# Optimization experiments

Hardware: AMD Instinct MI355X
Metric: run time of the kernel (lower is better)

Reference implementation:

```python
import jax, jax.numpy as jnp
import numpy as np

EMBED_DIM = 1024
NUM_HEADS = 16
HEAD_DIM = EMBED_DIM // NUM_HEADS


def setup_inputs() -> dict:
    key = jax.random.key(0)
    k1, k2, k3, k4 = jax.random.split(key, 4)
    scale = 1.0 / np.sqrt(EMBED_DIM)
    x = jax.random.normal(k1, (2, 2048, EMBED_DIM), dtype=jnp.float32)
    Wqkv = jax.random.normal(k2, (3 * EMBED_DIM, EMBED_DIM), dtype=jnp.float32) * scale
    Wproj = jax.random.normal(k3, (EMBED_DIM, EMBED_DIM), dtype=jnp.float32) * scale
    bproj = jax.random.normal(k4, (EMBED_DIM,), dtype=jnp.float32) * 0.01
    return {"x": x, "Wqkv": Wqkv, "Wproj": Wproj, "bproj": bproj}


def reference(x, Wqkv, Wproj, bproj):
    B, T, D = x.shape
    # QKV projection (torch Linear: x @ W.T), no bias
    qkv = jnp.einsum('btd,ed->bte', x, Wqkv)              # [B, T, 3D]
    qkv = qkv.reshape(B, T, 3, NUM_HEADS, HEAD_DIM)
    qkv = jnp.transpose(qkv, (2, 0, 3, 1, 4))             # [3, B, H, T, hd]
    q, k, v = qkv[0], qkv[1], qkv[2]
    # scaled dot-product attention (full matrix, as in source)
    dots = jnp.einsum('bhqd,bhkd->bhqk', q, k) / jnp.sqrt(jnp.asarray(HEAD_DIM, x.dtype))
    attn = jax.nn.softmax(dots, axis=-1)
    out = jnp.einsum('bhqk,bhkd->bhqd', attn, v)          # [B, H, T, hd]
    out = jnp.transpose(out, (0, 2, 1, 3)).reshape(B, T, D)
    # output projection with bias
    return jnp.einsum('btd,ed->bte', out, Wproj) + bproj
```

## Files before the change

### kernel.cpp

```cpp
#include <hip/hip_runtime.h>

typedef __attribute__((ext_vector_type(8))) short bf16x8;
typedef __attribute__((ext_vector_type(4))) float f32x4;
typedef __attribute__((ext_vector_type(4))) unsigned int u32x4;

#define MFMA16(a, b, c) __builtin_amdgcn_mfma_f32_16x16x32_bf16((a), (b), (c), 0, 0, 0)

__device__ __forceinline__ unsigned short f2bf(float f) {
    unsigned u = __builtin_bit_cast(unsigned, f);
    u = (u + 0x7fffu + ((u >> 16) & 1u)) >> 16;
    return (unsigned short)u;
}

__device__ __forceinline__ unsigned pack2(float lo, float hi) {
    return (unsigned)f2bf(lo) | ((unsigned)f2bf(hi) << 16);
}

__device__ __forceinline__ void gll16(const void* g, void* l) {
    __builtin_amdgcn_global_load_lds((__attribute__((address_space(1))) void*)g,
                                     (__attribute__((address_space(3))) void*)l,
                                     16, 0, 0);
}

__global__ __launch_bounds__(256) void castk(const float* __restrict__ in,
                                             unsigned short* __restrict__ out, int n) {
    int stride = gridDim.x * blockDim.x;
    for (int i = blockIdx.x * blockDim.x + threadIdx.x; i * 4 < n; i += stride) {
        float4 v = ((const float4*)in)[i];
        ushort4 o;
        o.x = f2bf(v.x); o.y = f2bf(v.y); o.z = f2bf(v.z); o.w = f2bf(v.w);
        ((ushort4*)out)[i] = o;
    }
}

template <int EPI>
__global__ __launch_bounds__(256) void gemm_bt(const unsigned short* __restrict__ A,
                                               const unsigned short* __restrict__ B,
                                               int K,
                                               unsigned short* __restrict__ qbuf,
                                               unsigned short* __restrict__ kbuf,
                                               unsigned short* __restrict__ vtb,
                                               float* __restrict__ outF,
                                               const float* __restrict__ bias) {
    __shared__ __align__(16) unsigned short As[128 * 32];
    __shared__ __align__(16) unsigned short Bs[128 * 32];
    const int tid = threadIdx.x;
    const int w = tid >> 6, l = tid & 63;
    const int g = l >> 4, cc = l & 15;
    const int wr = w >> 1, wc = w & 1;
    const int m0 = blockIdx.y * 128, n0 = blockIdx.x * 128;

    f32x4 acc[4][4];
#pragma unroll
    for (int i = 0; i < 4; ++i)
#pragma unroll
        for (int j = 0; j < 4; ++j) acc[i][j] = (f32x4){0.f, 0.f, 0.f, 0.f};

    const int srow = (l >> 2);
    const int skk = (l & 3) * 8;

    for (int k0 = 0; k0 < K; k0 += 32) {
#pragma unroll
        for (int ch = 0; ch < 2; ++ch) {
            int ci = ch * 4 + w;
            int row = ci * 16 + srow;
            gll16(A + (size_t)(m0 + row) * K + k0 + skk, &As[ci * 512]);
            gll16(B + (size_t)(n0 + row) * K + k0 + skk, &Bs[ci * 512]);
        }
        __syncthreads();
        bf16x8 af[4], bfr[4];
#pragma unroll
        for (int i = 0; i < 4; ++i) {
            af[i]  = *(const bf16x8*)&As[(wr * 64 + i * 16 + cc) * 32 + g * 8];
            bfr[i] = *(const bf16x8*)&Bs[(wc * 64 + i * 16 + cc) * 32 + g * 8];
        }
#pragma unroll
        for (int i = 0; i < 4; ++i)
#pragma unroll
            for (int j = 0; j < 4; ++j) acc[i][j] = MFMA16(af[i], bfr[j], acc[i][j]);
        __syncthreads();
    }

    if (EPI == 0) {
        const int which = n0 >> 10;
#pragma unroll
        for (int jn = 0; jn < 4; ++jn) {
            int n = n0 + wc * 64 + jn * 16 + cc;
            int hn = n & 1023;
            int h = hn >> 6, d = hn & 63;
#pragma unroll
            for (int i = 0; i < 4; ++i) {
#pragma unroll
                for (int j = 0; j < 4; ++j) {
                    int m = m0 + wr * 64 + i * 16 + g * 4 + j;
                    int b = m >> 11, t = m & 2047;
                    int bh = b * 16 + h;
                    float v = acc[i][jn][j];
                    if (which == 0) {
                        qbuf[((size_t)bh * 2048 + t) * 64 + d] = f2bf(v * 0.125f);
                    } else if (which == 1) {
                        kbuf[((size_t)bh * 2048 + t) * 64 + d] = f2bf(v);
                    } else {
                        vtb[((size_t)bh * 64 + d) * 2048 + t] = f2bf(v);
                    }
                }
            }
        }
    } else {
#pragma unroll
        for (int jn = 0; jn < 4; ++jn) {
            int n = n0 + wc * 64 + jn * 16 + cc;
            float bn = bias[n];
#pragma unroll
            for (int i = 0; i < 4; ++i) {
#pragma unroll
                for (int j = 0; j < 4; ++j) {
                    int m = m0 + wr * 64 + i * 16 + g * 4 + j;
                    outF[(size_t)m * 1024 + n] = acc[i][jn][j] + bn;
                }
            }
        }
    }
}

__global__ __launch_bounds__(256) void attn_kernel(const unsigned short* __restrict__ qb,
                                                   const unsigned short* __restrict__ kb,
                                                   const unsigned short* __restrict__ vtb,
                                                   unsigned short* __restrict__ ao) {
    __shared__ __align__(16) unsigned short smem[16384];
    const int bh = blockIdx.y;
    const int w = threadIdx.x >> 6, l = threadIdx.x & 63;
    const int g = l >> 4, cc = l & 15;
    const int q0 = blockIdx.x * 128 + w * 32;

    const unsigned short* qbase = qb + (size_t)bh * 2048 * 64;
    const unsigned short* kbase = kb + (size_t)bh * 2048 * 64;
    const unsigned short* vbase = vtb + (size_t)bh * 64 * 2048;

    const int sl8 = l >> 3, sl7 = l & 7;
    const int sperm = ((sl7 ^ sl8) * 8);

#define STAGE(bb, kk)                                                                        \
    do {                                                                                     \
        int base = (bb) * 8192;                                                              \
        gll16(kbase + (size_t)((kk) + w * 8 + sl8) * 64 + sperm, &smem[base + w * 512]);     \
        gll16(kbase + (size_t)((kk) + (w + 4) * 8 + sl8) * 64 + sperm,                       \
              &smem[base + (w + 4) * 512]);                                                  \
        gll16(vbase + (size_t)(w * 8 + sl8) * 2048 + (kk) + sperm,                           \
              &smem[base + 4096 + w * 512]);                                                 \
        gll16(vbase + (size_t)((w + 4) * 8 + sl8) * 2048 + (kk) + sperm,                     \
              &smem[base + 4096 + (w + 4) * 512]);                                           \
    } while (0)

    bf16x8 qf[2][2];
#pragma unroll
    for (int qt = 0; qt < 2; ++qt)
#pragma unroll
        for (int kh = 0; kh < 2; ++kh)
            qf[qt][kh] = *(const bf16x8*)(qbase + (size_t)(q0 + qt * 16 + cc) * 64 + kh * 32 + g * 8);

    float mrun[2] = {-INFINITY, -INFINITY};
    float lrun[2] = {0.f, 0.f};
    f32x4 acc[2][4];
#pragma unroll
    for (int qt = 0; qt < 2; ++qt)
#pragma unroll
        for (int dt = 0; dt < 4; ++dt) acc[qt][dt] = (f32x4){0.f, 0.f, 0.f, 0.f};

    const int swz = cc & 7;
    const int slo = (g & 1) * 32 + cc, shi = slo + 16;

    STAGE(0, 0);
    asm volatile("s_waitcnt vmcnt(0)" ::: "memory");
    __syncthreads();

    for (int t = 0; t < 32; ++t) {
        const int cb = t & 1;
        if (t + 1 < 32) STAGE(cb ^ 1, (t + 1) * 64);

        const unsigned short* Kb = &smem[cb * 8192];
        const unsigned short* Vb = &smem[cb * 8192 + 4096];

        bf16x8 kf[4][2];
#pragma unroll
        for (int kt = 0; kt < 4; ++kt)
#pragma unroll
            for (int kh = 0; kh < 2; ++kh)
                kf[kt][kh] = *(const bf16x8*)&Kb[(kt * 16 + cc) * 64 + (((kh * 4 + g) ^ swz) * 8)];

        f32x4 s[2][4];
#pragma unroll
        for (int qt = 0; qt < 2; ++qt)
#pragma unroll
            for (int kt = 0; kt < 4; ++kt) {
                f32x4 z = (f32x4){0.f, 0.f, 0.f, 0.f};
                z = MFMA16(kf[kt][0], qf[qt][0], z);
                z = MFMA16(kf[kt][1], qf[qt][1], z);
                s[qt][kt] = z;
            }

        u32x4 pf[2][2];
#pragma unroll
        for (int qt = 0; qt < 2; ++qt) {
            float mc = s[qt][0][0];
#pragma unroll
            for (int kt = 0; kt < 4; ++kt)
#pragma unroll
                for (int j = 0; j < 4; ++j) mc = fmaxf(mc, s[qt][kt][j]);
            mc = fmaxf(mc, __shfl_xor(mc, 16));
            mc = fmaxf(mc, __shfl_xor(mc, 32));
            float mnew = fmaxf(mrun[qt], mc);
            float fsc = __expf(mrun[qt] - mnew);
            mrun[qt] = mnew;
            float p[4][4], sum = 0.f;
#pragma unroll
            for (int kt = 0; kt < 4; ++kt)
#pragma unroll
                for (int j = 0; j < 4; ++j) {
                    p[kt][j] = __expf(s[qt][kt][j] - mnew);
                    sum += p[kt][j];
                }
            lrun[qt] = lrun[qt] * fsc + sum;
#pragma unroll
            for (int dt = 0; dt < 4; ++dt) acc[qt][dt] = acc[qt][dt] * fsc;

#pragma unroll
            for (int c = 0; c < 2; ++c) {
                unsigned b0 = pack2(p[2 * c][0], p[2 * c][1]);
                unsigned b1 = pack2(p[2 * c][2], p[2 * c][3]);
                unsigned b2 = pack2(p[2 * c + 1][0], p[2 * c + 1][1]);
                unsigned b3 = pack2(p[2 * c + 1][2], p[2 * c + 1][3]);
                unsigned a0 = (unsigned)__shfl((int)b0, slo), a1 = (unsigned)__shfl((int)b1, slo);
                unsigned a2 = (unsigned)__shfl((int)b0, shi), a3 = (unsigned)__shfl((int)b1, shi);
                unsigned d0 = (unsigned)__shfl((int)b2, slo), d1 = (unsigned)__shfl((int)b3, slo);
                unsigned d2 = (unsigned)__shfl((int)b2, shi), d3 = (unsigned)__shfl((int)b3, shi);
                u32x4 wv;
                if (g < 2) { wv.x = a0; wv.y = a1; wv.z = a2; wv.w = a3; }
                else       { wv.x = d0; wv.y = d1; wv.z = d2; wv.w = d3; }
                pf[qt][c] = wv;
            }
        }

#pragma unroll
        for (int c = 0; c < 2; ++c)
#pragma unroll
            for (int dt = 0; dt < 4; ++dt) {
                bf16x8 vf = *(const bf16x8*)&Vb[(dt * 16 + cc) * 64 + (((c * 4 + g) ^ swz) * 8)];
                acc[0][dt] = MFMA16(vf, __builtin_bit_cast(bf16x8, pf[0][c]), acc[0][dt]);
                acc[1][dt] = MFMA16(vf, __builtin_bit_cast(bf16x8, pf[1][c]), acc[1][dt]);
            }

        asm volatile("s_waitcnt vmcnt(0)" ::: "memory");
        __syncthreads();
    }
#undef STAGE

    const int b = bh >> 4, h = bh & 15;
#pragma unroll
    for (int qt = 0; qt < 2; ++qt) {
        float lsum = lrun[qt];
        lsum += __shfl_xor(lsum, 16);
        lsum += __shfl_xor(lsum, 32);
        float inv = 1.f / lsum;
        size_t rowbase = ((size_t)(b * 2048 + q0 + qt * 16 + cc)) * 1024 + h * 64;
#pragma unroll
        for (int dt = 0; dt < 4; ++dt)
#pragma unroll
            for (int j = 0; j < 4; ++j)
                ao[rowbase + dt * 16 + g * 4 + j] = f2bf(acc[qt][dt][j] * inv);
    }
}

extern "C" void kernel_launch(void* const* d_in, const int* in_sizes, int n_in,
                              void* d_out, int out_size, void* d_ws, size_t ws_size,
                              hipStream_t stream) {
    const float* x = (const float*)d_in[0];
    const float* Wqkv = (const float*)d_in[1];
    const float* Wproj = (const float*)d_in[2];
    const float* bproj = (const float*)d_in[3];
    float* out = (float*)d_out;

    unsigned short* xb = (unsigned short*)d_ws;
    unsigned short* wqkvb = xb + 4096 * 1024;
    unsigned short* wprojb = wqkvb + 3072 * 1024;
    unsigned short* qbuf = wprojb + 1024 * 1024;
    unsigned short* kbuf = qbuf + 32 * 2048 * 64;
    unsigned short* vtb = kbuf + 32 * 2048 * 64;
    unsigned short* aob = vtb + 32 * 2048 * 64;

    castk<<<1024, 256, 0, stream>>>(x, xb, 4096 * 1024);
    castk<<<1024, 256, 0, stream>>>(Wqkv, wqkvb, 3072 * 1024);
    castk<<<512, 256, 0, stream>>>(Wproj, wprojb, 1024 * 1024);

    gemm_bt<0><<<dim3(24, 32), 256, 0, stream>>>(xb, wqkvb, 1024, qbuf, kbuf, vtb, nullptr, nullptr);
    attn_kernel<<<dim3(16, 32), 256, 0, stream>>>(qbuf, kbuf, vtb, aob);
    gemm_bt<1><<<dim3(8, 32), 256, 0, stream>>>(aob, wprojb, 1024, nullptr, nullptr, nullptr, out, bproj);
}
```

Before: 231.5 us.

## Double-buffer GEMM loads, swizzle tile order, streamline attention softmax and PV MFMAs

```diff
diff --git a/kernel.cpp b/kernel.cpp
--- a/kernel.cpp
+++ b/kernel.cpp
@@ -1,10 +1,12 @@
 #include <hip/hip_runtime.h>
 
 typedef __attribute__((ext_vector_type(8))) short bf16x8;
+typedef __attribute__((ext_vector_type(4))) short bf16x4;
 typedef __attribute__((ext_vector_type(4))) float f32x4;
-typedef __attribute__((ext_vector_type(4))) unsigned int u32x4;
-
-#define MFMA16(a, b, c) __builtin_amdgcn_mfma_f32_16x16x32_bf16((a), (b), (c), 0, 0, 0)
+typedef __attribute__((ext_vector_type(2))) unsigned int u32x2;
+
+#define MFMA32(a, b, c) __builtin_amdgcn_mfma_f32_16x16x32_bf16((a), (b), (c), 0, 0, 0)
+#define MFMA16K(a, b, c) __builtin_amdgcn_mfma_f32_16x16x16bf16_1k((a), (b), (c), 0, 0, 0)
 
 __device__ __forceinline__ unsigned short f2bf(float f) {
     unsigned u = __builtin_bit_cast(unsigned, f);
@@ -12,8 +14,10 @@
     return (unsigned short)u;
 }
 
-__device__ __forceinline__ unsigned pack2(float lo, float hi) {
-    return (unsigned)f2bf(lo) | ((unsigned)f2bf(hi) << 16);
+__device__ __forceinline__ unsigned cvtpk(float lo, float hi) {
+    unsigned r;
+    asm("v_cvt_pk_bf16_f32 %0, %1, %2" : "=v"(r) : "v"(lo), "v"(hi));
+    return r;
 }
 
 __device__ __forceinline__ void gll16(const void* g, void* l) {
@@ -42,13 +46,18 @@
                                                unsigned short* __restrict__ vtb,
                                                float* __restrict__ outF,
                                                const float* __restrict__ bias) {
-    __shared__ __align__(16) unsigned short As[128 * 32];
-    __shared__ __align__(16) unsigned short Bs[128 * 32];
+    __shared__ __align__(16) unsigned short As[2][4096];
+    __shared__ __align__(16) unsigned short Bs[2][4096];
     const int tid = threadIdx.x;
     const int w = tid >> 6, l = tid & 63;
     const int g = l >> 4, cc = l & 15;
     const int wr = w >> 1, wc = w & 1;
-    const int m0 = blockIdx.y * 128, n0 = blockIdx.x * 128;
+
+    const int nwg = gridDim.x * gridDim.y;
+    const int lin = blockIdx.y * gridDim.x + blockIdx.x;
+    const int swz = (lin & 7) * (nwg >> 3) + (lin >> 3);
+    const int bx = swz % gridDim.x, by = swz / gridDim.x;
+    const int m0 = by * 128, n0 = bx * 128;
 
     f32x4 acc[4][4];
 #pragma unroll
@@ -59,27 +68,39 @@
     const int srow = (l >> 2);
     const int skk = (l & 3) * 8;
 
-    for (int k0 = 0; k0 < K; k0 += 32) {
-#pragma unroll
-        for (int ch = 0; ch < 2; ++ch) {
-            int ci = ch * 4 + w;
-            int row = ci * 16 + srow;
-            gll16(A + (size_t)(m0 + row) * K + k0 + skk, &As[ci * 512]);
-            gll16(B + (size_t)(n0 + row) * K + k0 + skk, &Bs[ci * 512]);
-        }
+#define GSTAGE(bb, k0)                                                          \
+    do {                                                                        \
+        _Pragma("unroll") for (int ch = 0; ch < 2; ++ch) {                      \
+            int ci = ch * 4 + w;                                                \
+            int row = ci * 16 + srow;                                           \
+            gll16(A + (size_t)(m0 + row) * K + (k0) + skk, &As[bb][ci * 512]);  \
+            gll16(B + (size_t)(n0 + row) * K + (k0) + skk, &Bs[bb][ci * 512]);  \
+        }                                                                       \
+    } while (0)
+
+    GSTAGE(0, 0);
+    asm volatile("s_waitcnt vmcnt(0)" ::: "memory");
+    __syncthreads();
+
+    const int nt = K >> 5;
+    int cur = 0;
+    for (int t = 0; t < nt; ++t) {
+        if (t + 1 < nt) GSTAGE(cur ^ 1, (t + 1) * 32);
+        bf16x8 af[4], bfr[4];
+#pragma unroll
+        for (int i = 0; i < 4; ++i) {
+            af[i]  = *(const bf16x8*)&As[cur][(wr * 64 + i * 16 + cc) * 32 + g * 8];
+            bfr[i] = *(const bf16x8*)&Bs[cur][(wc * 64 + i * 16 + cc) * 32 + g * 8];
+        }
+#pragma unroll
+        for (int i = 0; i < 4; ++i)
+#pragma unroll
+            for (int j = 0; j < 4; ++j) acc[i][j] = MFMA32(af[i], bfr[j], acc[i][j]);
+        asm volatile("s_waitcnt vmcnt(0)" ::: "memory");
         __syncthreads();
-        bf16x8 af[4], bfr[4];
-#pragma unroll
-        for (int i = 0; i < 4; ++i) {
-            af[i]  = *(const bf16x8*)&As[(wr * 64 + i * 16 + cc) * 32 + g * 8];
-            bfr[i] = *(const bf16x8*)&Bs[(wc * 64 + i * 16 + cc) * 32 + g * 8];
-        }
-#pragma unroll
-        for (int i = 0; i < 4; ++i)
-#pragma unroll
-            for (int j = 0; j < 4; ++j) acc[i][j] = MFMA16(af[i], bfr[j], acc[i][j]);
-        __syncthreads();
-    }
+        cur ^= 1;
+    }
+#undef GSTAGE
 
     if (EPI == 0) {
         const int which = n0 >> 10;
@@ -97,7 +118,7 @@
                     int bh = b * 16 + h;
                     float v = acc[i][jn][j];
                     if (which == 0) {
-                        qbuf[((size_t)bh * 2048 + t) * 64 + d] = f2bf(v * 0.125f);
+                        qbuf[((size_t)bh * 2048 + t) * 64 + d] = f2bf(v * 0.1803368801f);
                     } else if (which == 1) {
                         kbuf[((size_t)bh * 2048 + t) * 64 + d] = f2bf(v);
                     } else {
@@ -168,7 +189,6 @@
         for (int dt = 0; dt < 4; ++dt) acc[qt][dt] = (f32x4){0.f, 0.f, 0.f, 0.f};
 
     const int swz = cc & 7;
-    const int slo = (g & 1) * 32 + cc, shi = slo + 16;
 
     STAGE(0, 0);
     asm volatile("s_waitcnt vmcnt(0)" ::: "memory");
@@ -189,17 +209,19 @@
                 kf[kt][kh] = *(const bf16x8*)&Kb[(kt * 16 + cc) * 64 + (((kh * 4 + g) ^ swz) * 8)];
 
         f32x4 s[2][4];
+        __builtin_amdgcn_s_setprio(1);
 #pragma unroll
         for (int qt = 0; qt < 2; ++qt)
 #pragma unroll
             for (int kt = 0; kt < 4; ++kt) {
                 f32x4 z = (f32x4){0.f, 0.f, 0.f, 0.f};
-                z = MFMA16(kf[kt][0], qf[qt][0], z);
-                z = MFMA16(kf[kt][1], qf[qt][1], z);
+                z = MFMA32(kf[kt][0], qf[qt][0], z);
+                z = MFMA32(kf[kt][1], qf[qt][1], z);
                 s[qt][kt] = z;
             }
-
-        u32x4 pf[2][2];
+        __builtin_amdgcn_s_setprio(0);
+
+        bf16x4 pf[2][4];
 #pragma unroll
         for (int qt = 0; qt < 2; ++qt) {
             float mc = s[qt][0][0];
@@ -210,45 +232,41 @@
             mc = fmaxf(mc, __shfl_xor(mc, 16));
             mc = fmaxf(mc, __shfl_xor(mc, 32));
             float mnew = fmaxf(mrun[qt], mc);
-            float fsc = __expf(mrun[qt] - mnew);
+            float fsc = __builtin_amdgcn_exp2f(mrun[qt] - mnew);
             mrun[qt] = mnew;
-            float p[4][4], sum = 0.f;
+            float sum = 0.f;
 #pragma unroll
             for (int kt = 0; kt < 4; ++kt)
 #pragma unroll
                 for (int j = 0; j < 4; ++j) {
-                    p[kt][j] = __expf(s[qt][kt][j] - mnew);
-                    sum += p[kt][j];
+                    float pv = __builtin_amdgcn_exp2f(s[qt][kt][j] - mnew);
+                    s[qt][kt][j] = pv;
+                    sum += pv;
                 }
             lrun[qt] = lrun[qt] * fsc + sum;
 #pragma unroll
             for (int dt = 0; dt < 4; ++dt) acc[qt][dt] = acc[qt][dt] * fsc;
-
-#pragma unroll
-            for (int c = 0; c < 2; ++c) {
-                unsigned b0 = pack2(p[2 * c][0], p[2 * c][1]);
-                unsigned b1 = pack2(p[2 * c][2], p[2 * c][3]);
-                unsigned b2 = pack2(p[2 * c + 1][0], p[2 * c + 1][1]);
-                unsigned b3 = pack2(p[2 * c + 1][2], p[2 * c + 1][3]);
-                unsigned a0 = (unsigned)__shfl((int)b0, slo), a1 = (unsigned)__shfl((int)b1, slo);
-                unsigned a2 = (unsigned)__shfl((int)b0, shi), a3 = (unsigned)__shfl((int)b1, shi);
-                unsigned d0 = (unsigned)__shfl((int)b2, slo), d1 = (unsigned)__shfl((int)b3, slo);
-                unsigned d2 = (unsigned)__shfl((int)b2, shi), d3 = (unsigned)__shfl((int)b3, shi);
-                u32x4 wv;
-                if (g < 2) { wv.x = a0; wv.y = a1; wv.z = a2; wv.w = a3; }
-                else       { wv.x = d0; wv.y = d1; wv.z = d2; wv.w = d3; }
-                pf[qt][c] = wv;
-            }
-        }
-
-#pragma unroll
-        for (int c = 0; c < 2; ++c)
+#pragma unroll
+            for (int kt = 0; kt < 4; ++kt) {
+                u32x2 wv;
+                wv.x = cvtpk(s[qt][kt][0], s[qt][kt][1]);
+                wv.y = cvtpk(s[qt][kt][2], s[qt][kt][3]);
+                pf[qt][kt] = __builtin_bit_cast(bf16x4, wv);
+            }
+        }
+
+        __builtin_amdgcn_s_setprio(1);
+#pragma unroll
+        for (int kt = 0; kt < 4; ++kt) {
+            const int seg = ((kt * 2 + (g >> 1)) ^ swz);
 #pragma unroll
             for (int dt = 0; dt < 4; ++dt) {
-                bf16x8 vf = *(const bf16x8*)&Vb[(dt * 16 + cc) * 64 + (((c * 4 + g) ^ swz) * 8)];
-                acc[0][dt] = MFMA16(vf, __builtin_bit_cast(bf16x8, pf[0][c]), acc[0][dt]);
-                acc[1][dt] = MFMA16(vf, __builtin_bit_cast(bf16x8, pf[1][c]), acc[1][dt]);
-            }
+                bf16x4 vf = *(const bf16x4*)&Vb[(dt * 16 + cc) * 64 + seg * 8 + (g & 1) * 4];
+                acc[0][dt] = MFMA16K(vf, pf[0][kt], acc[0][dt]);
+                acc[1][dt] = MFMA16K(vf, pf[1][kt], acc[1][dt]);
+            }
+        }
+        __builtin_amdgcn_s_setprio(0);
 
         asm volatile("s_waitcnt vmcnt(0)" ::: "memory");
         __syncthreads();
@@ -264,10 +282,12 @@
         float inv = 1.f / lsum;
         size_t rowbase = ((size_t)(b * 2048 + q0 + qt * 16 + cc)) * 1024 + h * 64;
 #pragma unroll
-        for (int dt = 0; dt < 4; ++dt)
-#pragma unroll
-            for (int j = 0; j < 4; ++j)
-                ao[rowbase + dt * 16 + g * 4 + j] = f2bf(acc[qt][dt][j] * inv);
+        for (int dt = 0; dt < 4; ++dt) {
+            u32x2 ov;
+            ov.x = cvtpk(acc[qt][dt][0] * inv, acc[qt][dt][1] * inv);
+            ov.y = cvtpk(acc[qt][dt][2] * inv, acc[qt][dt][3] * inv);
+            *(u32x2*)(ao + rowbase + dt * 16 + g * 4) = ov;
+        }
     }
 }
 
```

Result: faster. 212.0 us (-8.4%).
